# Performance work log

Hardware: AMD Instinct MI355X
Metric: run time of the kernel (lower is better)

The kernel has to match this reference:

```python
import jax, jax.numpy as jnp
import numpy as np

SCALES = (2, 4, 8)  # primitive_scales, one per branch


def setup_inputs() -> dict:
    key = jax.random.key(0)
    k0, k1, k2, k3, k4 = jax.random.split(key, 5)
    B, C, H, W = 16, 256, 128, 128
    s = 1.0 / np.sqrt(C).astype(np.float32)
    return {
        "x": jax.random.normal(k0, (B, C, H, W), jnp.float32),
        "W_proto": jax.random.normal(k1, (3, C, C), jnp.float32) * s,
        "W_frame": jax.random.normal(k2, (3, C, C), jnp.float32) * s,
        "W_out": jax.random.normal(k3, (3, C, C), jnp.float32) * s,
        "W_fuse": jax.random.normal(k4, (C, 3 * C), jnp.float32) * (1.0 / np.sqrt(3 * C).astype(np.float32)),
    }


def _branch(x, Wp, Wf, Wo, P):
    # x: [B,C,H,W]; adaptive_avg_pool2d(x, (H, P)) with W % P == 0 == mean over equal bins along W
    B, C, H, W = x.shape
    proto = x.reshape(B, C, H, P, W // P).mean(axis=-1)        # [B,C,H,P]
    proto = jnp.einsum('oc,bchp->bohp', Wp, proto)             # proto_proj (1x1 conv)
    q = jnp.einsum('oc,bchw->bhwo', Wf, x)                     # frame_proj + permute -> [B,H,W,C]
    # att = q @ k, k = proto.permute(0,2,1,3) -> [B,H,C,P]
    att = jnp.einsum('bhwc,bchp->bhwp', q, proto) * (1.0 / jnp.sqrt(jnp.float32(C)))
    att = jax.nn.softmax(att, axis=-1)                         # [B,H,W,P]
    # v = proto.permute(0,2,3,1) -> [B,H,P,C]; msg = att @ v -> [B,H,W,C]
    msg = jnp.einsum('bhwp,bchp->bhwc', att, proto)
    return jnp.einsum('oc,bhwc->bohw', Wo, msg)                # out_proj -> [B,C,H,W]


def reference(x, W_proto, W_frame, W_out, W_fuse):
    outs = [_branch(x, W_proto[i], W_frame[i], W_out[i], SCALES[i]) for i in range(len(SCALES))]
    cat = jnp.concatenate(outs, axis=1)                        # [B, 3C, H, W]
    return jnp.einsum('oc,bchw->bohw', W_fuse, cat) + x
```

## Files before the change

### kernel.cpp

```cpp
#include <hip/hip_runtime.h>
#include <hip/hip_bf16.h>
#include <math.h>
#include <stdint.h>

#define CC   256
#define HW   (128*128)
#define MAT  (CC*CC)
#define NBH  2048
#define N0   4096
#define N1   8192
#define N2   16384

typedef __attribute__((ext_vector_type(8))) short bf16x8;
typedef __attribute__((ext_vector_type(4))) float f32x4;
typedef __attribute__((address_space(3))) uint32_t lds_u32_t;
typedef __attribute__((address_space(1))) const uint32_t glb_u32_t;

__global__ __launch_bounds__(256) void k_mats1(
    const float* __restrict__ Wp, const float* __restrict__ Wf,
    const float* __restrict__ Wo, const float* __restrict__ Wfu,
    __hip_bfloat16* __restrict__ A, float* __restrict__ E)
{
    int idx = blockIdx.x;
    int t = threadIdx.x;
    if (idx < 3*CC) {
        int i = idx >> 8, c = idx & 255;
        const float* wf = Wf + (size_t)i*MAT;
        const float* wp = Wp + (size_t)i*MAT;
        float acc = 0.f;
        for (int o = 0; o < CC; ++o)
            acc += wf[o*CC + c] * wp[o*CC + t];
        A[(size_t)i*512*CC + (size_t)c*CC + t] = __float2bfloat16(acc);
    } else {
        idx -= 3*CC;
        int i = idx >> 8, o = idx & 255;
        const float* wo = Wo + (size_t)i*MAT;
        const float* wfu = Wfu + (size_t)o*(3*CC) + i*CC;
        float acc = 0.f;
        for (int c3 = 0; c3 < CC; ++c3)
            acc += wfu[c3] * wo[c3*CC + t];
        E[(size_t)i*MAT + (size_t)o*CC + t] = acc;
    }
}

__global__ __launch_bounds__(256) void k_mats2(
    const float* __restrict__ Wp, const float* __restrict__ E,
    __hip_bfloat16* __restrict__ A)
{
    int idx = blockIdx.x;
    int i = idx >> 8, o = idx & 255;
    int t = threadIdx.x;
    const float* e = E + (size_t)i*MAT + (size_t)o*CC;
    const float* wp = Wp + (size_t)i*MAT;
    float acc = 0.f;
    for (int c = 0; c < CC; ++c)
        acc += e[c] * wp[c*CC + t];
    A[(size_t)i*512*CC + (size_t)(256+o)*CC + t] = __float2bfloat16(acc);
}

__global__ __launch_bounds__(256, 4) void k_poolA(
    const float* __restrict__ x, float* __restrict__ binsG)
{
    int bc = blockIdx.x;
    int t = threadIdx.x;
    const float4* xp = (const float4*)(x + (size_t)bc*HW) + t;
    __shared__ float bins[128][9];
    float4 v[16];
    #pragma unroll
    for (int i = 0; i < 16; ++i) v[i] = xp[i*256];
    int hb = t >> 5, bin = (t & 31) >> 2;
    #pragma unroll
    for (int i = 0; i < 16; ++i) {
        float s = v[i].x + v[i].y + v[i].z + v[i].w;
        s += __shfl_xor(s, 1);
        s += __shfl_xor(s, 2);
        if ((t & 3) == 0) bins[i*8 + hb][bin] = s;
    }
    __syncthreads();
    int h = t >> 1, b0 = (t & 1) * 4;
    float4 o;
    o.x = bins[h][b0+0]; o.y = bins[h][b0+1];
    o.z = bins[h][b0+2]; o.w = bins[h][b0+3];
    ((float4*)binsG)[(size_t)bc*256 + t] = o;
}

__global__ __launch_bounds__(256) void k_poolB(
    const float* __restrict__ binsG, __hip_bfloat16* __restrict__ Bt)
{
    int bh = blockIdx.x;
    int b = bh >> 7, h = bh & 127;
    int c = threadIdx.x;
    const float* g = binsG + (((size_t)b*256 + c)*128 + h)*8;
    float4 lo = *(const float4*)(g);
    float4 hi = *(const float4*)(g + 4);
    float b8[8] = {lo.x, lo.y, lo.z, lo.w, hi.x, hi.y, hi.z, hi.w};

    __hip_bfloat16* B0 = Bt;
    __hip_bfloat16* B1 = Bt + (size_t)N0*CC;
    __hip_bfloat16* B2 = Bt + (size_t)(N0+N1)*CC;
    B0[((size_t)bh*2 + 0)*CC + c] = __float2bfloat16((b8[0]+b8[1]+b8[2]+b8[3]) * (1.f/64.f));
    B0[((size_t)bh*2 + 1)*CC + c] = __float2bfloat16((b8[4]+b8[5]+b8[6]+b8[7]) * (1.f/64.f));
    #pragma unroll
    for (int j = 0; j < 4; ++j)
        B1[((size_t)bh*4 + j)*CC + c] = __float2bfloat16((b8[2*j]+b8[2*j+1]) * (1.f/32.f));
    #pragma unroll
    for (int j = 0; j < 8; ++j)
        B2[((size_t)bh*8 + j)*CC + c] = __float2bfloat16(b8[j] * (1.f/16.f));
}

__global__ __launch_bounds__(128) void k_gemm(
    const __hip_bfloat16* __restrict__ A,
    const __hip_bfloat16* __restrict__ Bt,
    __hip_bfloat16* __restrict__ Cc)
{
    int blk = blockIdx.x;
    int br, lb, LP, poff;
    if (blk < 256)      { br = 0; lb = blk;       LP = 1; poff = 0; }
    else if (blk < 768) { br = 1; lb = blk - 256; LP = 2; poff = 2; }
    else                { br = 2; lb = blk - 768; LP = 3; poff = 6; }
    size_t aoff  = (size_t)br*512*CC;
    size_t btoff = (br == 0) ? 0 : (br == 1 ? (size_t)N0*CC : (size_t)(N0+N1)*CC);
    const __hip_bfloat16* Ab = A  + aoff;
    const __hip_bfloat16* Bb = Bt + btoff;

    int rb = lb & 3, cb = lb >> 2;
    int wv = threadIdx.x >> 6, lane = threadIdx.x & 63;
    int row0 = rb*128 + wv*64;
    int col0 = cb*64;
    int lr = lane & 15, lk = (lane >> 4) * 8;

    f32x4 acc[4][4] = {};
    for (int kk = 0; kk < CC; kk += 32) {
        bf16x8 af[4], bfr[4];
        #pragma unroll
        for (int m = 0; m < 4; ++m)
            af[m] = *reinterpret_cast<const bf16x8*>(Ab + (size_t)(row0 + m*16 + lr)*CC + kk + lk);
        #pragma unroll
        for (int n = 0; n < 4; ++n)
            bfr[n] = *reinterpret_cast<const bf16x8*>(Bb + (size_t)(col0 + n*16 + lr)*CC + kk + lk);
        #pragma unroll
        for (int m = 0; m < 4; ++m)
            #pragma unroll
            for (int n = 0; n < 4; ++n)
                acc[m][n] = __builtin_amdgcn_mfma_f32_16x16x32_bf16(af[m], bfr[n], acc[m][n], 0, 0, 0);
    }

    int cr = (lane >> 4) * 4, ccol = lane & 15;
    int pm = (1 << LP) - 1;
    #pragma unroll
    for (int m = 0; m < 4; ++m) {
        #pragma unroll
        for (int n = 0; n < 4; ++n) {
            int colg = col0 + n*16 + ccol;
            int bh = colg >> LP, p = colg & pm;
            __hip_bfloat16* dst = Cc + (size_t)bh*8192 + poff + p;
            #pragma unroll
            for (int j = 0; j < 4; ++j) {
                int r = row0 + m*16 + cr + j;
                dst[r*16] = __float2bfloat16(acc[m][n][j]);
            }
        }
    }
}

template<int L>
__device__ __forceinline__ void softmax2(float2* a) {
    float mx = a[0].x, my = a[0].y;
    #pragma unroll
    for (int j = 1; j < L; ++j) { mx = fmaxf(mx, a[j].x); my = fmaxf(my, a[j].y); }
    float sx = 0.f, sy = 0.f;
    #pragma unroll
    for (int j = 0; j < L; ++j) {
        a[j].x = __expf(a[j].x - mx); sx += a[j].x;
        a[j].y = __expf(a[j].y - my); sy += a[j].y;
    }
    float rx = 1.f / sx, ry = 1.f / sy;
    #pragma unroll
    for (int j = 0; j < L; ++j) { a[j].x *= rx; a[j].y *= ry; }
}

__global__ __launch_bounds__(256, 4) void k_main(
    const float* __restrict__ x, const __hip_bfloat16* __restrict__ Cc,
    float* __restrict__ out)
{
    int bh = blockIdx.x;
    int b = bh >> 7, h = bh & 127;
    int t = threadIdx.x;
    int lane = t & 63;
    int wv = __builtin_amdgcn_readfirstlane(t >> 6);
    const uint32_t* Cb = (const uint32_t*)(Cc + (size_t)bh*8192);
    const float* xg = x  + ((size_t)b*CC)*HW + h*128;
    float*       og = out + ((size_t)b*CC)*HW + h*128;

    __shared__ float xbuf[4][32*128];
    __shared__ float att_sx[2][64][15];
    __shared__ float att_sy[2][64][15];

    float2 att[14];
    #pragma unroll
    for (int p = 0; p < 14; ++p) att[p] = make_float2(0.f, 0.f);

    auto STAGE = [&](int tt) {
        int cb = (tt & 7) * 32;
        float* bufp = xbuf[tt & 3];
        #pragma unroll
        for (int q = 0; q < 4; ++q) {
            int c0 = cb + wv*8 + q*2;
            const float* gp = xg + (size_t)(c0 + (lane >> 5))*HW + (lane & 31)*4;
            float* lp = &bufp[(wv*8 + q*2)*128];
            __builtin_amdgcn_global_load_lds((glb_u32_t*)gp, (lds_u32_t*)lp, 16, 0, 0);
        }
    };

    STAGE(0);
    STAGE(1);
    STAGE(2);

    #pragma unroll 1
    for (int tt = 0; tt < 16; ++tt) {
        if (tt == 8) {
            if (wv >= 2) {
                #pragma unroll
                for (int p = 0; p < 14; ++p) {
                    att_sx[wv-2][lane][p] = att[p].x;
                    att_sy[wv-2][lane][p] = att[p].y;
                }
            }
            __syncthreads();
            if (wv < 2) {
                #pragma unroll
                for (int p = 0; p < 14; ++p) {
                    att[p].x += att_sx[wv][lane][p];
                    att[p].y += att_sy[wv][lane][p];
                }
                if (wv == 1) {
                    #pragma unroll
                    for (int p = 0; p < 14; ++p) {
                        att_sx[1][lane][p] = att[p].x;
                        att_sy[1][lane][p] = att[p].y;
                    }
                }
            }
            __syncthreads();
            if (wv == 0) {
                #pragma unroll
                for (int p = 0; p < 14; ++p) {
                    att[p].x = (att[p].x + att_sx[1][lane][p]) * 0.0625f;
                    att[p].y = (att[p].y + att_sy[1][lane][p]) * 0.0625f;
                }
                softmax2<2>(att + 0);
                softmax2<4>(att + 2);
                softmax2<8>(att + 6);
                #pragma unroll
                for (int p = 0; p < 14; ++p) {
                    att_sx[0][lane][p] = att[p].x;
                    att_sy[0][lane][p] = att[p].y;
                }
            }
            __syncthreads();
            #pragma unroll
            for (int p = 0; p < 14; ++p) {
                att[p].x = att_sx[0][lane][p];
                att[p].y = att_sy[0][lane][p];
            }
        }

        if (tt < 8)       asm volatile("s_waitcnt vmcnt(8)"  ::: "memory");
        else if (tt < 14) asm volatile("s_waitcnt vmcnt(16)" ::: "memory");
        else if (tt == 14) asm volatile("s_waitcnt vmcnt(12)" ::: "memory");
        else               asm volatile("s_waitcnt vmcnt(8)"  ::: "memory");
        __builtin_amdgcn_sched_barrier(0);

        if (tt + 3 < 16) STAGE(tt + 3);

        {
            int cb = (tt & 7) * 32;
            bool passB = (tt >= 8);
            const float* xb = &xbuf[tt & 3][(wv*8)*128];
            int crow = (passB ? 256 : 0) + cb + wv*8;
            const uint32_t* wr = Cb + (size_t)crow*8;
            #pragma unroll
            for (int half = 0; half < 2; ++half) {
                uint32_t u[4][7];
                #pragma unroll
                for (int q = 0; q < 4; ++q)
                    #pragma unroll
                    for (int j = 0; j < 7; ++j)
                        u[q][j] = wr[(half*4 + q)*8 + j];
                #pragma unroll
                for (int q = 0; q < 4; ++q) {
                    int qq = half*4 + q;
                    float2 xv = *(const float2*)&xb[qq*128 + lane*2];
                    if (!passB) {
                        #pragma unroll
                        for (int j = 0; j < 7; ++j) {
                            float mlo = __uint_as_float(u[q][j] << 16);
                            float mhi = __uint_as_float(u[q][j] & 0xFFFF0000u);
                            att[2*j].x   += xv.x * mlo;  att[2*j].y   += xv.y * mlo;
                            att[2*j+1].x += xv.x * mhi;  att[2*j+1].y += xv.y * mhi;
                        }
                    } else {
                        float2 acc = xv;
                        #pragma unroll
                        for (int j = 0; j < 7; ++j) {
                            float vlo = __uint_as_float(u[q][j] << 16);
                            float vhi = __uint_as_float(u[q][j] & 0xFFFF0000u);
                            acc.x += att[2*j].x * vlo;   acc.y += att[2*j].y * vlo;
                            acc.x += att[2*j+1].x * vhi; acc.y += att[2*j+1].y * vhi;
                        }
                        int o = cb + wv*8 + qq;
                        *(float2*)&og[(size_t)o*HW + lane*2] = acc;
                    }
                }
            }
        }
    }
}

extern "C" void kernel_launch(void* const* d_in, const int* in_sizes, int n_in,
                              void* d_out, int out_size, void* d_ws, size_t ws_size,
                              hipStream_t stream)
{
    (void)in_sizes; (void)n_in; (void)out_size; (void)ws_size;
    const float* x   = (const float*)d_in[0];
    const float* Wp  = (const float*)d_in[1];
    const float* Wf  = (const float*)d_in[2];
    const float* Wo  = (const float*)d_in[3];
    const float* Wfu = (const float*)d_in[4];
    float* out = (float*)d_out;

    char* wsb = (char*)d_ws;
    float*          E     = (float*)wsb;
    __hip_bfloat16* A     = (__hip_bfloat16*)(wsb + 786432);
    __hip_bfloat16* Bt    = (__hip_bfloat16*)(wsb + 1572864);
    __hip_bfloat16* Cc    = (__hip_bfloat16*)(wsb + 16252928);
    float*          binsG = (float*)(wsb + 16252928);

    k_mats1<<<dim3(6*CC),  dim3(256), 0, stream>>>(Wp, Wf, Wo, Wfu, A, E);
    k_mats2<<<dim3(3*CC),  dim3(256), 0, stream>>>(Wp, E, A);
    k_poolA<<<dim3(4096),  dim3(256), 0, stream>>>(x, binsG);
    k_poolB<<<dim3(NBH),   dim3(256), 0, stream>>>(binsG, Bt);
    k_gemm <<<dim3(1792),  dim3(128), 0, stream>>>(A, Bt, Cc);
    k_main <<<dim3(NBH),   dim3(256), 0, stream>>>(x, Cc, out);
}
```

Measured before the change: 326.8 us.

## Assign one row per wave in k_main to drop cross-wave attention reduction

k_main now processes four H rows per block, with each wave owning a full row and iterating over all channels in 8-channel stages. The cross-wave LDS reduction of attention logits and the broadcast of softmax results go away, along with two __syncthreads, because each wave holds its complete logits. The cost is four times as many serial iterations per wave, a per-iteration s_barrier, a grid cut from 2048 to 512 blocks, and more outstanding loads to track through vmcnt.

Measured after the change: 336.7 us. 3.0% more time.

```diff
diff --git a/kernel.cpp b/kernel.cpp
--- a/kernel.cpp
+++ b/kernel.cpp
@@ -179,36 +179,39 @@
     for (int j = 0; j < L; ++j) { a[j].x *= rx; a[j].y *= ry; }
 }
 
-__global__ __launch_bounds__(256, 4) void k_main(
+__global__ __launch_bounds__(256, 2) void k_main(
     const float* __restrict__ x, const __hip_bfloat16* __restrict__ Cc,
     float* __restrict__ out)
 {
-    int bh = blockIdx.x;
-    int b = bh >> 7, h = bh & 127;
+    int blk = blockIdx.x;
+    int b = blk >> 5, hq = blk & 31;
+    int h0 = hq * 4;
     int t = threadIdx.x;
     int lane = t & 63;
     int wv = __builtin_amdgcn_readfirstlane(t >> 6);
+    int bh = b*128 + h0 + wv;
     const uint32_t* Cb = (const uint32_t*)(Cc + (size_t)bh*8192);
-    const float* xg = x  + ((size_t)b*CC)*HW + h*128;
-    float*       og = out + ((size_t)b*CC)*HW + h*128;
-
-    __shared__ float xbuf[4][32*128];
-    __shared__ float att_sx[2][64][15];
-    __shared__ float att_sy[2][64][15];
+    const float* xg = x   + ((size_t)b*CC)*HW + h0*128;
+    float*       og = out + ((size_t)b*CC)*HW + h0*128;
+
+    __shared__ float xbuf[4][8*512];
 
     float2 att[14];
     #pragma unroll
     for (int p = 0; p < 14; ++p) att[p] = make_float2(0.f, 0.f);
 
     auto STAGE = [&](int tt) {
-        int cb = (tt & 7) * 32;
+        int cb = (tt & 31) * 8;
         float* bufp = xbuf[tt & 3];
         #pragma unroll
-        for (int q = 0; q < 4; ++q) {
-            int c0 = cb + wv*8 + q*2;
-            const float* gp = xg + (size_t)(c0 + (lane >> 5))*HW + (lane & 31)*4;
-            float* lp = &bufp[(wv*8 + q*2)*128];
-            __builtin_amdgcn_global_load_lds((glb_u32_t*)gp, (lds_u32_t*)lp, 16, 0, 0);
+        for (int e = 0; e < 2; ++e) {
+            int c = cb + wv*2 + e;
+            #pragma unroll
+            for (int q = 0; q < 2; ++q) {
+                const float* gp = xg + (size_t)c*HW + q*256 + lane*4;
+                float* lp = &bufp[(wv*2 + e)*512 + q*256];
+                __builtin_amdgcn_global_load_lds((glb_u32_t*)gp, (lds_u32_t*)lp, 16, 0, 0);
+            }
         }
     };
 
@@ -217,67 +220,34 @@
     STAGE(2);
 
     #pragma unroll 1
-    for (int tt = 0; tt < 16; ++tt) {
-        if (tt == 8) {
-            if (wv >= 2) {
-                #pragma unroll
-                for (int p = 0; p < 14; ++p) {
-                    att_sx[wv-2][lane][p] = att[p].x;
-                    att_sy[wv-2][lane][p] = att[p].y;
-                }
+    for (int tt = 0; tt < 64; ++tt) {
+        if (tt == 32) {
+            #pragma unroll
+            for (int p = 0; p < 14; ++p) {
+                att[p].x *= 0.0625f;
+                att[p].y *= 0.0625f;
             }
-            __syncthreads();
-            if (wv < 2) {
-                #pragma unroll
-                for (int p = 0; p < 14; ++p) {
-                    att[p].x += att_sx[wv][lane][p];
-                    att[p].y += att_sy[wv][lane][p];
-                }
-                if (wv == 1) {
-                    #pragma unroll
-                    for (int p = 0; p < 14; ++p) {
-                        att_sx[1][lane][p] = att[p].x;
-                        att_sy[1][lane][p] = att[p].y;
-                    }
-                }
-            }
-            __syncthreads();
-            if (wv == 0) {
-                #pragma unroll
-                for (int p = 0; p < 14; ++p) {
-                    att[p].x = (att[p].x + att_sx[1][lane][p]) * 0.0625f;
-                    att[p].y = (att[p].y + att_sy[1][lane][p]) * 0.0625f;
-                }
-                softmax2<2>(att + 0);
-                softmax2<4>(att + 2);
-                softmax2<8>(att + 6);
-                #pragma unroll
-                for (int p = 0; p < 14; ++p) {
-                    att_sx[0][lane][p] = att[p].x;
-                    att_sy[0][lane][p] = att[p].y;
-                }
-            }
-            __syncthreads();
-            #pragma unroll
-            for (int p = 0; p < 14; ++p) {
-                att[p].x = att_sx[0][lane][p];
-                att[p].y = att_sy[0][lane][p];
-            }
+            softmax2<2>(att + 0);
+            softmax2<4>(att + 2);
+            softmax2<8>(att + 6);
         }
 
-        if (tt < 8)       asm volatile("s_waitcnt vmcnt(8)"  ::: "memory");
-        else if (tt < 14) asm volatile("s_waitcnt vmcnt(16)" ::: "memory");
-        else if (tt == 14) asm volatile("s_waitcnt vmcnt(12)" ::: "memory");
-        else               asm volatile("s_waitcnt vmcnt(8)"  ::: "memory");
+        if (tt < 33)       asm volatile("s_waitcnt vmcnt(8)"  ::: "memory");
+        else if (tt == 33) asm volatile("s_waitcnt vmcnt(16)" ::: "memory");
+        else if (tt == 34) asm volatile("s_waitcnt vmcnt(24)" ::: "memory");
+        else if (tt <= 61) asm volatile("s_waitcnt vmcnt(32)" ::: "memory");
+        else if (tt == 62) asm volatile("s_waitcnt vmcnt(28)" ::: "memory");
+        else               asm volatile("s_waitcnt vmcnt(24)" ::: "memory");
         __builtin_amdgcn_sched_barrier(0);
-
-        if (tt + 3 < 16) STAGE(tt + 3);
+        __builtin_amdgcn_s_barrier();
+
+        if (tt + 3 < 64) STAGE(tt + 3);
 
         {
-            int cb = (tt & 7) * 32;
-            bool passB = (tt >= 8);
-            const float* xb = &xbuf[tt & 3][(wv*8)*128];
-            int crow = (passB ? 256 : 0) + cb + wv*8;
+            int cb = (tt & 31) * 8;
+            bool passB = (tt >= 32);
+            const float* xb = xbuf[tt & 3];
+            int crow = (passB ? 256 : 0) + cb;
             const uint32_t* wr = Cb + (size_t)crow*8;
             #pragma unroll
             for (int half = 0; half < 2; ++half) {
@@ -289,8 +259,8 @@
                         u[q][j] = wr[(half*4 + q)*8 + j];
                 #pragma unroll
                 for (int q = 0; q < 4; ++q) {
-                    int qq = half*4 + q;
-                    float2 xv = *(const float2*)&xb[qq*128 + lane*2];
+                    int s = half*4 + q;
+                    float2 xv = *(const float2*)&xb[s*512 + wv*128 + lane*2];
                     if (!passB) {
                         #pragma unroll
                         for (int j = 0; j < 7; ++j) {
@@ -308,8 +278,8 @@
                             acc.x += att[2*j].x * vlo;   acc.y += att[2*j].y * vlo;
                             acc.x += att[2*j+1].x * vhi; acc.y += att[2*j+1].y * vhi;
                         }
-                        int o = cb + wv*8 + qq;
-                        *(float2*)&og[(size_t)o*HW + lane*2] = acc;
+                        int o = cb + s;
+                        *(float2*)&og[(size_t)o*HW + wv*128 + lane*2] = acc;
                     }
                 }
             }
@@ -341,5 +311,5 @@
     k_poolA<<<dim3(4096),  dim3(256), 0, stream>>>(x, binsG);
     k_poolB<<<dim3(NBH),   dim3(256), 0, stream>>>(binsG, Bt);
     k_gemm <<<dim3(1792),  dim3(128), 0, stream>>>(A, Bt, Cc);
-    k_main <<<dim3(NBH),   dim3(256), 0, stream>>>(x, Cc, out);
-}
+    k_main <<<dim3(512),   dim3(256), 0, stream>>>(x, Cc, out);
+}
```

## Pre-cast input to bf16 and feed pooling and main kernels from it

Applied to the files above, without the earlier changes.

Adds a kernel that converts x to bf16 in a large workspace buffer. Bf16 variants of the pooling and main kernels then read half-size data and stage it into half-size LDS tiles. The goal is to cut global and LDS bandwidth in the two heavy readers of x. The cost is an extra full pass that reads x and writes the bf16 copy, so total memory traffic may rise. The residual add now also uses the bf16-rounded x, which loses precision. The fp32 path is kept as a fallback when the workspace is too small.

New measurement: 341.2 us. 4.4% more time.

```diff
diff --git a/kernel.cpp b/kernel.cpp
--- a/kernel.cpp
+++ b/kernel.cpp
@@ -15,6 +15,23 @@
 typedef __attribute__((ext_vector_type(4))) float f32x4;
 typedef __attribute__((address_space(3))) uint32_t lds_u32_t;
 typedef __attribute__((address_space(1))) const uint32_t glb_u32_t;
+
+__global__ __launch_bounds__(256) void k_cast(
+    const float4* __restrict__ x4, ushort4* __restrict__ xb4)
+{
+    int idx = blockIdx.x * 256 + threadIdx.x;
+    int stride = gridDim.x * 256;
+    #pragma unroll 4
+    for (int i = idx; i < 16777216; i += stride) {
+        float4 v = x4[i];
+        union { __hip_bfloat16 h[4]; ushort4 u; } c;
+        c.h[0] = __float2bfloat16(v.x);
+        c.h[1] = __float2bfloat16(v.y);
+        c.h[2] = __float2bfloat16(v.z);
+        c.h[3] = __float2bfloat16(v.w);
+        xb4[i] = c.u;
+    }
+}
 
 __global__ __launch_bounds__(256) void k_mats1(
     const float* __restrict__ Wp, const float* __restrict__ Wf,
@@ -58,7 +75,7 @@
     A[(size_t)i*512*CC + (size_t)(256+o)*CC + t] = __float2bfloat16(acc);
 }
 
-__global__ __launch_bounds__(256, 4) void k_poolA(
+__global__ __launch_bounds__(256, 4) void k_poolA_f32(
     const float* __restrict__ x, float* __restrict__ binsG)
 {
     int bc = blockIdx.x;
@@ -72,6 +89,35 @@
     #pragma unroll
     for (int i = 0; i < 16; ++i) {
         float s = v[i].x + v[i].y + v[i].z + v[i].w;
+        s += __shfl_xor(s, 1);
+        s += __shfl_xor(s, 2);
+        if ((t & 3) == 0) bins[i*8 + hb][bin] = s;
+    }
+    __syncthreads();
+    int h = t >> 1, b0 = (t & 1) * 4;
+    float4 o;
+    o.x = bins[h][b0+0]; o.y = bins[h][b0+1];
+    o.z = bins[h][b0+2]; o.w = bins[h][b0+3];
+    ((float4*)binsG)[(size_t)bc*256 + t] = o;
+}
+
+__global__ __launch_bounds__(256, 4) void k_poolA_bf(
+    const __hip_bfloat16* __restrict__ xb, float* __restrict__ binsG)
+{
+    int bc = blockIdx.x;
+    int t = threadIdx.x;
+    const ushort4* xp = (const ushort4*)(xb + (size_t)bc*HW) + t;
+    __shared__ float bins[128][9];
+    ushort4 v[16];
+    #pragma unroll
+    for (int i = 0; i < 16; ++i) v[i] = xp[i*256];
+    int hb = t >> 5, bin = (t & 31) >> 2;
+    #pragma unroll
+    for (int i = 0; i < 16; ++i) {
+        float s = __uint_as_float((uint32_t)v[i].x << 16)
+                + __uint_as_float((uint32_t)v[i].y << 16)
+                + __uint_as_float((uint32_t)v[i].z << 16)
+                + __uint_as_float((uint32_t)v[i].w << 16);
         s += __shfl_xor(s, 1);
         s += __shfl_xor(s, 2);
         if ((t & 3) == 0) bins[i*8 + hb][bin] = s;
@@ -179,7 +225,150 @@
     for (int j = 0; j < L; ++j) { a[j].x *= rx; a[j].y *= ry; }
 }
 
-__global__ __launch_bounds__(256, 4) void k_main(
+__global__ __launch_bounds__(256, 4) void k_main_bf(
+    const __hip_bfloat16* __restrict__ xb, const __hip_bfloat16* __restrict__ Cc,
+    float* __restrict__ out)
+{
+    int bh = blockIdx.x;
+    int b = bh >> 7, h = bh & 127;
+    int t = threadIdx.x;
+    int lane = t & 63;
+    int wv = __builtin_amdgcn_readfirstlane(t >> 6);
+    const uint32_t* Cb = (const uint32_t*)(Cc + (size_t)bh*8192);
+    const __hip_bfloat16* xg = xb + ((size_t)b*CC)*HW + h*128;
+    float2* o2 = (float2*)out + ((size_t)b*CC)*(HW/2) + h*64 + lane;
+
+    __shared__ __hip_bfloat16 xbuf[4][32*128];
+    __shared__ float att_sx[2][64][15];
+    __shared__ float att_sy[2][64][15];
+
+    float2 att[14];
+    #pragma unroll
+    for (int p = 0; p < 14; ++p) att[p] = make_float2(0.f, 0.f);
+
+    auto STAGE = [&](int tt) {
+        int cb = (tt & 7) * 32;
+        __hip_bfloat16* bufp = xbuf[tt & 3];
+        #pragma unroll
+        for (int e = 0; e < 2; ++e) {
+            int c0 = cb + wv*8 + e*4;
+            const __hip_bfloat16* gp = xg + (size_t)(c0 + (lane >> 4))*HW + (lane & 15)*8;
+            __hip_bfloat16* lp = &bufp[(wv*8 + e*4)*128];
+            __builtin_amdgcn_global_load_lds((glb_u32_t*)gp, (lds_u32_t*)lp, 16, 0, 0);
+        }
+    };
+
+    STAGE(0);
+    STAGE(1);
+    STAGE(2);
+
+    #pragma unroll 1
+    for (int tt = 0; tt < 16; ++tt) {
+        if (tt == 8) {
+            if (wv >= 2) {
+                #pragma unroll
+                for (int p = 0; p < 14; ++p) {
+                    att_sx[wv-2][lane][p] = att[p].x;
+                    att_sy[wv-2][lane][p] = att[p].y;
+                }
+            }
+            __syncthreads();
+            if (wv < 2) {
+                #pragma unroll
+                for (int p = 0; p < 14; ++p) {
+                    att[p].x += att_sx[wv][lane][p];
+                    att[p].y += att_sy[wv][lane][p];
+                }
+                if (wv == 1) {
+                    #pragma unroll
+                    for (int p = 0; p < 14; ++p) {
+                        att_sx[1][lane][p] = att[p].x;
+                        att_sy[1][lane][p] = att[p].y;
+                    }
+                }
+            }
+            __syncthreads();
+            if (wv == 0) {
+                #pragma unroll
+                for (int p = 0; p < 14; ++p) {
+                    att[p].x = (att[p].x + att_sx[1][lane][p]) * 0.0625f;
+                    att[p].y = (att[p].y + att_sy[1][lane][p]) * 0.0625f;
+                }
+                softmax2<2>(att + 0);
+                softmax2<4>(att + 2);
+                softmax2<8>(att + 6);
+                #pragma unroll
+                for (int p = 0; p < 14; ++p) {
+                    att_sx[0][lane][p] = att[p].x;
+                    att_sy[0][lane][p] = att[p].y;
+                }
+            }
+            __syncthreads();
+            #pragma unroll
+            for (int p = 0; p < 14; ++p) {
+                att[p].x = att_sx[0][lane][p];
+                att[p].y = att_sy[0][lane][p];
+            }
+        }
+
+        if (tt <= 8)       asm volatile("s_waitcnt vmcnt(4)"  ::: "memory");
+        else if (tt == 9)  asm volatile("s_waitcnt vmcnt(12)" ::: "memory");
+        else if (tt == 10) asm volatile("s_waitcnt vmcnt(20)" ::: "memory");
+        else if (tt <= 13) asm volatile("s_waitcnt vmcnt(28)" ::: "memory");
+        else if (tt == 14) asm volatile("s_waitcnt vmcnt(26)" ::: "memory");
+        else               asm volatile("s_waitcnt vmcnt(24)" ::: "memory");
+        __builtin_amdgcn_sched_barrier(0);
+
+        if (tt + 3 < 16) STAGE(tt + 3);
+
+        {
+            int cb = (tt & 7) * 32;
+            bool passB = (tt >= 8);
+            const uint32_t* xrow = (const uint32_t*)&xbuf[tt & 3][(wv*8)*128];
+            int crow = (passB ? 256 : 0) + cb + wv*8;
+            const uint32_t* wr = Cb + (size_t)crow*8;
+            #pragma unroll
+            for (int half = 0; half < 2; ++half) {
+                uint32_t u[4][7];
+                #pragma unroll
+                for (int q = 0; q < 4; ++q)
+                    #pragma unroll
+                    for (int j = 0; j < 7; ++j)
+                        u[q][j] = wr[(half*4 + q)*8 + j];
+                #pragma unroll
+                for (int q = 0; q < 4; ++q) {
+                    int qq = half*4 + q;
+                    uint32_t xu = xrow[qq*64 + lane];
+                    float2 xv;
+                    xv.x = __uint_as_float(xu << 16);
+                    xv.y = __uint_as_float(xu & 0xFFFF0000u);
+                    if (!passB) {
+                        #pragma unroll
+                        for (int j = 0; j < 7; ++j) {
+                            float mlo = __uint_as_float(u[q][j] << 16);
+                            float mhi = __uint_as_float(u[q][j] & 0xFFFF0000u);
+                            att[2*j].x   += xv.x * mlo;  att[2*j].y   += xv.y * mlo;
+                            att[2*j+1].x += xv.x * mhi;  att[2*j+1].y += xv.y * mhi;
+                        }
+                    } else {
+                        float2 acc = xv;
+                        #pragma unroll
+                        for (int j = 0; j < 7; ++j) {
+                            float vlo = __uint_as_float(u[q][j] << 16);
+                            float vhi = __uint_as_float(u[q][j] & 0xFFFF0000u);
+                            acc.x += att[2*j].x * vlo;   acc.y += att[2*j].y * vlo;
+                            acc.x += att[2*j+1].x * vhi; acc.y += att[2*j+1].y * vhi;
+                        }
+                        int o = cb + wv*8 + qq;
+                        o2[(size_t)o*(HW/2)] = acc;
+                    }
+                }
+            }
+        }
+    }
+}
+
+__global__ __launch_bounds__(256, 4) void k_main_f32(
     const float* __restrict__ x, const __hip_bfloat16* __restrict__ Cc,
     float* __restrict__ out)
 {
@@ -212,9 +401,7 @@
         }
     };
 
-    STAGE(0);
-    STAGE(1);
-    STAGE(2);
+    STAGE(0); STAGE(1); STAGE(2);
 
     #pragma unroll 1
     for (int tt = 0; tt < 16; ++tt) {
@@ -276,7 +463,7 @@
         {
             int cb = (tt & 7) * 32;
             bool passB = (tt >= 8);
-            const float* xb = &xbuf[tt & 3][(wv*8)*128];
+            const float* xbuf_w = &xbuf[tt & 3][(wv*8)*128];
             int crow = (passB ? 256 : 0) + cb + wv*8;
             const uint32_t* wr = Cb + (size_t)crow*8;
             #pragma unroll
@@ -290,7 +477,7 @@
                 #pragma unroll
                 for (int q = 0; q < 4; ++q) {
                     int qq = half*4 + q;
-                    float2 xv = *(const float2*)&xb[qq*128 + lane*2];
+                    float2 xv = *(const float2*)&xbuf_w[qq*128 + lane*2];
                     if (!passB) {
                         #pragma unroll
                         for (int j = 0; j < 7; ++j) {
@@ -321,7 +508,7 @@
                               void* d_out, int out_size, void* d_ws, size_t ws_size,
                               hipStream_t stream)
 {
-    (void)in_sizes; (void)n_in; (void)out_size; (void)ws_size;
+    (void)in_sizes; (void)n_in; (void)out_size;
     const float* x   = (const float*)d_in[0];
     const float* Wp  = (const float*)d_in[1];
     const float* Wf  = (const float*)d_in[2];
@@ -335,11 +522,23 @@
     __hip_bfloat16* Bt    = (__hip_bfloat16*)(wsb + 1572864);
     __hip_bfloat16* Cc    = (__hip_bfloat16*)(wsb + 16252928);
     float*          binsG = (float*)(wsb + 16252928);
-
-    k_mats1<<<dim3(6*CC),  dim3(256), 0, stream>>>(Wp, Wf, Wo, Wfu, A, E);
-    k_mats2<<<dim3(3*CC),  dim3(256), 0, stream>>>(Wp, E, A);
-    k_poolA<<<dim3(4096),  dim3(256), 0, stream>>>(x, binsG);
-    k_poolB<<<dim3(NBH),   dim3(256), 0, stream>>>(binsG, Bt);
-    k_gemm <<<dim3(1792),  dim3(128), 0, stream>>>(A, Bt, Cc);
-    k_main <<<dim3(NBH),   dim3(256), 0, stream>>>(x, Cc, out);
-}
+    __hip_bfloat16* xbf   = (__hip_bfloat16*)(wsb + 49807360);
+
+    const size_t NEED_BIG = 49807360u + 134217728u;
+
+    k_mats1<<<dim3(6*CC), dim3(256), 0, stream>>>(Wp, Wf, Wo, Wfu, A, E);
+    k_mats2<<<dim3(3*CC), dim3(256), 0, stream>>>(Wp, E, A);
+
+    if (ws_size >= NEED_BIG) {
+        k_cast   <<<dim3(2048), dim3(256), 0, stream>>>((const float4*)x, (ushort4*)xbf);
+        k_poolA_bf<<<dim3(4096), dim3(256), 0, stream>>>(xbf, binsG);
+        k_poolB  <<<dim3(NBH),  dim3(256), 0, stream>>>(binsG, Bt);
+        k_gemm   <<<dim3(1792), dim3(128), 0, stream>>>(A, Bt, Cc);
+        k_main_bf<<<dim3(NBH),  dim3(256), 0, stream>>>(xbf, Cc, out);
+    } else {
+        k_poolA_f32<<<dim3(4096), dim3(256), 0, stream>>>(x, binsG);
+        k_poolB  <<<dim3(NBH),  dim3(256), 0, stream>>>(binsG, Bt);
+        k_gemm   <<<dim3(1792), dim3(128), 0, stream>>>(A, Bt, Cc);
+        k_main_f32<<<dim3(NBH), dim3(256), 0, stream>>>(x, Cc, out);
+    }
+}
```

## Split GEMM output into per-branch buffers with LDS-staged coalesced writes

Applied to the files above, without the earlier changes.

The GEMM epilogue used to scatter single bf16 values into an interleaved [bh][512][16] buffer with a stride of 16 elements, so its stores were uncoalesced. Each result tile is now staged through LDS and written out as vector stores into three separate per-branch buffers (2, 4 and 8 columns per row). The main kernel then reads each row as a uint32, uint2 and uint4 load instead of seven scalar loads. This adds LDS use in the GEMM and splits the per-row weight fetch into three separate streams in the main kernel.

Measured after the change: 354.9 us. 8.6% more time.

```diff
diff --git a/kernel.cpp b/kernel.cpp
--- a/kernel.cpp
+++ b/kernel.cpp
@@ -111,13 +111,15 @@
 __global__ __launch_bounds__(128) void k_gemm(
     const __hip_bfloat16* __restrict__ A,
     const __hip_bfloat16* __restrict__ Bt,
-    __hip_bfloat16* __restrict__ Cc)
+    __hip_bfloat16* __restrict__ C0,
+    __hip_bfloat16* __restrict__ C1,
+    __hip_bfloat16* __restrict__ C2)
 {
     int blk = blockIdx.x;
-    int br, lb, LP, poff;
-    if (blk < 256)      { br = 0; lb = blk;       LP = 1; poff = 0; }
-    else if (blk < 768) { br = 1; lb = blk - 256; LP = 2; poff = 2; }
-    else                { br = 2; lb = blk - 768; LP = 3; poff = 6; }
+    int br, lb;
+    if (blk < 256)      { br = 0; lb = blk;       }
+    else if (blk < 768) { br = 1; lb = blk - 256; }
+    else                { br = 2; lb = blk - 768; }
     size_t aoff  = (size_t)br*512*CC;
     size_t btoff = (br == 0) ? 0 : (br == 1 ? (size_t)N0*CC : (size_t)(N0+N1)*CC);
     const __hip_bfloat16* Ab = A  + aoff;
@@ -145,20 +147,42 @@
                 acc[m][n] = __builtin_amdgcn_mfma_f32_16x16x32_bf16(af[m], bfr[n], acc[m][n], 0, 0, 0);
     }
 
+    __shared__ ushort tile[2][64][68];
+    ushort (*tl)[68] = tile[wv];
     int cr = (lane >> 4) * 4, ccol = lane & 15;
-    int pm = (1 << LP) - 1;
-    #pragma unroll
-    for (int m = 0; m < 4; ++m) {
-        #pragma unroll
-        for (int n = 0; n < 4; ++n) {
-            int colg = col0 + n*16 + ccol;
-            int bh = colg >> LP, p = colg & pm;
-            __hip_bfloat16* dst = Cc + (size_t)bh*8192 + poff + p;
+    #pragma unroll
+    for (int m = 0; m < 4; ++m)
+        #pragma unroll
+        for (int n = 0; n < 4; ++n)
             #pragma unroll
             for (int j = 0; j < 4; ++j) {
-                int r = row0 + m*16 + cr + j;
-                dst[r*16] = __float2bfloat16(acc[m][n][j]);
-            }
+                __hip_bfloat16 hv = __float2bfloat16(acc[m][n][j]);
+                tl[m*16 + cr + j][n*16 + ccol] = *(ushort*)&hv;
+            }
+
+    int r = row0 + lane;
+    if (br == 2) {
+        #pragma unroll
+        for (int ch = 0; ch < 8; ++ch) {
+            int bh = cb*8 + ch;
+            uint2 a = *(const uint2*)&tl[lane][ch*8];
+            uint2 b = *(const uint2*)&tl[lane][ch*8 + 4];
+            uint4 v; v.x = a.x; v.y = a.y; v.z = b.x; v.w = b.y;
+            *(uint4*)(C2 + ((size_t)bh*512 + r)*8) = v;
+        }
+    } else if (br == 1) {
+        #pragma unroll
+        for (int ch = 0; ch < 16; ++ch) {
+            int bh = cb*16 + ch;
+            uint2 v = *(const uint2*)&tl[lane][ch*4];
+            *(uint2*)(C1 + ((size_t)bh*512 + r)*4) = v;
+        }
+    } else {
+        #pragma unroll
+        for (int ch = 0; ch < 32; ++ch) {
+            int bh = cb*32 + ch;
+            uint32_t v = *(const uint32_t*)&tl[lane][ch*2];
+            *(uint32_t*)(C0 + ((size_t)bh*512 + r)*2) = v;
         }
     }
 }
@@ -179,8 +203,24 @@
     for (int j = 0; j < L; ++j) { a[j].x *= rx; a[j].y *= ry; }
 }
 
+__device__ __forceinline__ void fma14(
+    float2* att, float2 xv, uint32_t w0, uint2 w1, uint4 w2)
+{
+    uint32_t u[7] = {w0, w1.x, w1.y, w2.x, w2.y, w2.z, w2.w};
+    #pragma unroll
+    for (int p = 0; p < 7; ++p) {
+        float lo = __uint_as_float(u[p] << 16);
+        float hi = __uint_as_float(u[p] & 0xFFFF0000u);
+        att[2*p].x   += xv.x * lo;  att[2*p].y   += xv.y * lo;
+        att[2*p+1].x += xv.x * hi;  att[2*p+1].y += xv.y * hi;
+    }
+}
+
 __global__ __launch_bounds__(256, 4) void k_main(
-    const float* __restrict__ x, const __hip_bfloat16* __restrict__ Cc,
+    const float* __restrict__ x,
+    const __hip_bfloat16* __restrict__ C0,
+    const __hip_bfloat16* __restrict__ C1,
+    const __hip_bfloat16* __restrict__ C2,
     float* __restrict__ out)
 {
     int bh = blockIdx.x;
@@ -188,7 +228,9 @@
     int t = threadIdx.x;
     int lane = t & 63;
     int wv = __builtin_amdgcn_readfirstlane(t >> 6);
-    const uint32_t* Cb = (const uint32_t*)(Cc + (size_t)bh*8192);
+    const uint32_t* C0b = (const uint32_t*)C0 + (size_t)bh*512;
+    const uint2*    C1b = (const uint2*)   C1 + (size_t)bh*512;
+    const uint4*    C2b = (const uint4*)   C2 + (size_t)bh*512;
     const float* xg = x  + ((size_t)b*CC)*HW + h*128;
     float*       og = out + ((size_t)b*CC)*HW + h*128;
 
@@ -212,9 +254,7 @@
         }
     };
 
-    STAGE(0);
-    STAGE(1);
-    STAGE(2);
+    STAGE(0); STAGE(1); STAGE(2);
 
     #pragma unroll 1
     for (int tt = 0; tt < 16; ++tt) {
@@ -277,40 +317,28 @@
             int cb = (tt & 7) * 32;
             bool passB = (tt >= 8);
             const float* xb = &xbuf[tt & 3][(wv*8)*128];
-            int crow = (passB ? 256 : 0) + cb + wv*8;
-            const uint32_t* wr = Cb + (size_t)crow*8;
+            int crow0 = (passB ? 256 : 0) + cb + wv*8;
             #pragma unroll
-            for (int half = 0; half < 2; ++half) {
-                uint32_t u[4][7];
-                #pragma unroll
-                for (int q = 0; q < 4; ++q)
+            for (int q = 0; q < 8; ++q) {
+                int crow = crow0 + q;
+                uint32_t w0 = C0b[crow];
+                uint2    w1 = C1b[crow];
+                uint4    w2 = C2b[crow];
+                float2 xv = *(const float2*)&xb[q*128 + lane*2];
+                if (!passB) {
+                    fma14(att, xv, w0, w1, w2);
+                } else {
+                    float2 acc = xv;
+                    uint32_t u[7] = {w0, w1.x, w1.y, w2.x, w2.y, w2.z, w2.w};
                     #pragma unroll
-                    for (int j = 0; j < 7; ++j)
-                        u[q][j] = wr[(half*4 + q)*8 + j];
-                #pragma unroll
-                for (int q = 0; q < 4; ++q) {
-                    int qq = half*4 + q;
-                    float2 xv = *(const float2*)&xb[qq*128 + lane*2];
-                    if (!passB) {
-                        #pragma unroll
-                        for (int j = 0; j < 7; ++j) {
-                            float mlo = __uint_as_float(u[q][j] << 16);
-                            float mhi = __uint_as_float(u[q][j] & 0xFFFF0000u);
-                            att[2*j].x   += xv.x * mlo;  att[2*j].y   += xv.y * mlo;
-                            att[2*j+1].x += xv.x * mhi;  att[2*j+1].y += xv.y * mhi;
-                        }
-                    } else {
-                        float2 acc = xv;
-                        #pragma unroll
-                        for (int j = 0; j < 7; ++j) {
-                            float vlo = __uint_as_float(u[q][j] << 16);
-                            float vhi = __uint_as_float(u[q][j] & 0xFFFF0000u);
-                            acc.x += att[2*j].x * vlo;   acc.y += att[2*j].y * vlo;
-                            acc.x += att[2*j+1].x * vhi; acc.y += att[2*j+1].y * vhi;
-                        }
-                        int o = cb + wv*8 + qq;
-                        *(float2*)&og[(size_t)o*HW + lane*2] = acc;
+                    for (int p = 0; p < 7; ++p) {
+                        float vlo = __uint_as_float(u[p] << 16);
+                        float vhi = __uint_as_float(u[p] & 0xFFFF0000u);
+                        acc.x += att[2*p].x * vlo + att[2*p+1].x * vhi;
+                        acc.y += att[2*p].y * vlo + att[2*p+1].y * vhi;
                     }
+                    int o = cb + wv*8 + q;
+                    *(float2*)&og[(size_t)o*HW + lane*2] = acc;
                 }
             }
         }
@@ -333,13 +361,15 @@
     float*          E     = (float*)wsb;
     __hip_bfloat16* A     = (__hip_bfloat16*)(wsb + 786432);
     __hip_bfloat16* Bt    = (__hip_bfloat16*)(wsb + 1572864);
-    __hip_bfloat16* Cc    = (__hip_bfloat16*)(wsb + 16252928);
     float*          binsG = (float*)(wsb + 16252928);
-
-    k_mats1<<<dim3(6*CC),  dim3(256), 0, stream>>>(Wp, Wf, Wo, Wfu, A, E);
-    k_mats2<<<dim3(3*CC),  dim3(256), 0, stream>>>(Wp, E, A);
-    k_poolA<<<dim3(4096),  dim3(256), 0, stream>>>(x, binsG);
-    k_poolB<<<dim3(NBH),   dim3(256), 0, stream>>>(binsG, Bt);
-    k_gemm <<<dim3(1792),  dim3(128), 0, stream>>>(A, Bt, Cc);
-    k_main <<<dim3(NBH),   dim3(256), 0, stream>>>(x, Cc, out);
-}
+    __hip_bfloat16* C0    = (__hip_bfloat16*)(wsb + 33030144);
+    __hip_bfloat16* C1    = (__hip_bfloat16*)(wsb + 37224448);
+    __hip_bfloat16* C2    = (__hip_bfloat16*)(wsb + 45613056);
+
+    k_mats1<<<dim3(6*CC), dim3(256), 0, stream>>>(Wp, Wf, Wo, Wfu, A, E);
+    k_mats2<<<dim3(3*CC), dim3(256), 0, stream>>>(Wp, E, A);
+    k_poolA<<<dim3(4096), dim3(256), 0, stream>>>(x, binsG);
+    k_poolB<<<dim3(NBH),  dim3(256), 0, stream>>>(binsG, Bt);
+    k_gemm <<<dim3(1792), dim3(128), 0, stream>>>(A, Bt, C0, C1, C2);
+    k_main <<<dim3(NBH),  dim3(256), 0, stream>>>(x, C0, C1, C2, out);
+}
```
